# Performance work log

Hardware: AMD Instinct MI355X
Metric: run time of the kernel (lower is better)

The kernel has to match this reference:

```python
import jax, jax.numpy as jnp
import numpy as np

B, K, W = 16, 64, 2048
D, DH, DFF, NL, V = 512, 256, 2048, 4, 32001
LN_EPS = 1e-5


def _ln(x, g, b):
    mu = jnp.mean(x, axis=-1, keepdims=True)
    var = jnp.mean(jnp.square(x - mu), axis=-1, keepdims=True)
    return (x - mu) * jax.lax.rsqrt(var + LN_EPS) * g + b


def setup_inputs() -> dict:
    key = jax.random.key(0)
    ks = iter(jax.random.split(key, 64))
    nrm = lambda shape, s=0.02: (jax.random.normal(next(ks), shape, dtype=jnp.float32) * s)
    inp = {
        "cache": jax.random.randint(next(ks), (B, K), 0, V),
        "seq": jax.random.randint(next(ks), (B, W), 0, V),
        "item_embed": nrm((V, D)),
        "cache_pos_embed": nrm((K, D)),
        "seq_pos_embed": nrm((W, D)),
        "segment_embed": nrm((2, D)),
        # per-layer stacked params (leading dim NL)
        "wq_s": nrm((NL, D, DH)), "wk_s": nrm((NL, D, DH)), "wv_s": nrm((NL, D, DH)),
        "wq_c": nrm((NL, D, DH)), "wk_c": nrm((NL, D, DH)), "wv_c": nrm((NL, D, DH)),
        "w_out": nrm((NL, D, D)), "b_out": jnp.zeros((NL, D), jnp.float32),
        "ln1_g": jnp.ones((NL, D), jnp.float32), "ln1_b": jnp.zeros((NL, D), jnp.float32),
        "ln2_g": jnp.ones((NL, D), jnp.float32), "ln2_b": jnp.zeros((NL, D), jnp.float32),
        "w_ff1": nrm((NL, D, DFF)), "b_ff1": jnp.zeros((NL, DFF), jnp.float32),
        "w_ff2": nrm((NL, DFF, D)), "b_ff2": jnp.zeros((NL, D), jnp.float32),
        "fin_g": jnp.ones((D,), jnp.float32), "fin_b": jnp.zeros((D,), jnp.float32),
        "w_ev": nrm((D, 1)), "b_ev": jnp.zeros((1,), jnp.float32),
    }
    return inp


def _forward(cache, seq, item_embed, cache_pos_embed, seq_pos_embed, segment_embed,
             wq_s, wk_s, wv_s, wq_c, wk_c, wv_c, w_out, b_out,
             ln1_g, ln1_b, ln2_g, ln2_b, w_ff1, b_ff1, w_ff2, b_ff2,
             fin_g, fin_b, w_ev, b_ev):
    scale = 1.0 / jnp.sqrt(jnp.float32(DH))
    cache_emb = item_embed[cache] + cache_pos_embed[None, :, :] + segment_embed[0]
    seq_emb = item_embed[seq] + seq_pos_embed[None, :, :] + segment_embed[1]
    h = jnp.concatenate([cache_emb, seq_emb], axis=1)  # (B, K+W, D)
    L = K + W
    # additive mask for stream a: cache rows attend to all seq tokens,
    # seq rows are causal within the window.  (L, W)
    causal = jnp.triu(jnp.full((W, W), -jnp.inf, dtype=jnp.float32), k=1)
    mask_a = jnp.concatenate([jnp.zeros((K, W), jnp.float32), causal], axis=0)

    for l in range(NL):
        hn = _ln(h, ln1_g[l], ln1_b[l])
        hn_seq = hn[:, K:]
        hn_cache = hn[:, :K]
        # stream a: all tokens query the sequence window (causal for seq rows)
        q_a = hn @ wq_s[l]
        k_a = hn_seq @ wk_s[l]
        v_a = hn_seq @ wv_s[l]
        scores_a = jnp.einsum('bld,bwd->blw', q_a, k_a) * scale + mask_a
        out_a = jnp.einsum('blw,bwd->bld', jax.nn.softmax(scores_a, axis=-1), v_a)
        # stream b: all tokens query the cache slots (full attention)
        q_b = hn @ wq_c[l]
        k_b = hn_cache @ wk_c[l]
        v_b = hn_cache @ wv_c[l]
        scores_b = jnp.einsum('bld,bkd->blk', q_b, k_b) * scale
        out_b = jnp.einsum('blk,bkd->bld', jax.nn.softmax(scores_b, axis=-1), v_b)
        attn_out = jnp.concatenate([out_a, out_b], axis=-1)  # (B, L, D)
        h = h + attn_out @ w_out[l] + b_out[l]
        hn2 = _ln(h, ln2_g[l], ln2_b[l])
        h = h + jax.nn.relu(hn2 @ w_ff1[l] + b_ff1[l]) @ w_ff2[l] + b_ff2[l]

    h = _ln(h, fin_g, fin_b)
    logits = (h[:, :K] @ w_ev + b_ev)[..., 0]  # (B, K)
    return logits


def reference(cache, seq, item_embed, cache_pos_embed, seq_pos_embed, segment_embed,
              wq_s, wk_s, wv_s, wq_c, wk_c, wv_c, w_out, b_out,
              ln1_g, ln1_b, ln2_g, ln2_b, w_ff1, b_ff1, w_ff2, b_ff2,
              fin_g, fin_b, w_ev, b_ev):
    return _forward(cache, seq, item_embed, cache_pos_embed, seq_pos_embed, segment_embed,
                    wq_s, wk_s, wv_s, wq_c, wk_c, wv_c, w_out, b_out,
                    ln1_g, ln1_b, ln2_g, ln2_b, w_ff1, b_ff1, w_ff2, b_ff2,
                    fin_g, fin_b, w_ev, b_ev)
```

## Files before the change

### kernel.cpp

```cpp
#include <hip/hip_runtime.h>
#include <hip/hip_bf16.h>
#include <cstdint>

#define CB 16
#define CK 64
#define CW 2048
#define CL 2112
#define CD 512
#define CDH 256
#define CDFF 2048
#define CNL 4
#define CROWS (CB*CL)
#define RCH (CROWS/4)

typedef __attribute__((ext_vector_type(8))) short bf16x8;
typedef __attribute__((ext_vector_type(4))) float f32x4;

__device__ __forceinline__ float bf2f(unsigned short u) {
    union { unsigned int i; float f; } x; x.i = ((unsigned int)u) << 16; return x.f;
}

__device__ __forceinline__ void load_lds16(const void* g, void* l) {
    __builtin_amdgcn_global_load_lds(
        (const __attribute__((address_space(1))) void*)g,
        (__attribute__((address_space(3))) void*)l, 16, 0, 0);
}

__device__ __forceinline__ void xcd_swizzle(int& bx, int& by) {
    const int gx = gridDim.x, nwg = gx * gridDim.y;
    if ((nwg & 7) == 0) {
        const int flat = by * gx + bx;
        const int cpx = nwg >> 3;
        const int swz = (flat & 7) * cpx + (flat >> 3);
        bx = swz % gx; by = swz / gx;
    }
}

#define BM 128
#define BN 128
#define BKG 64

__global__ __launch_bounds__(256) void gemm_bt(
    const short* __restrict__ A, const short* __restrict__ Bt, void* __restrict__ C,
    const float* __restrict__ bias, int M, int N, int Kd,
    int lda, int ldb, int ldc, long sA, long sB, long sC, float scale, int epi,
    int ksplit)
{
    __shared__ short lA[2][BM * BKG];
    __shared__ short lB[2][BN * BKG];
    const int tid = threadIdx.x;
    const int wave = tid >> 6, lane = tid & 63;
    const int wy = wave >> 1, wx = wave & 1;
    const int lr = lane & 15, quad = lane >> 4;
    int bx = blockIdx.x, by = blockIdx.y;
    xcd_swizzle(bx, by);
    const int m0 = by * BM, n0 = bx * BN;
    const int z = blockIdx.z;
    const short* Ab = A + (size_t)z * sA;
    const short* Bb = Bt + (size_t)z * sB;

    f32x4 acc[4][4];
#pragma unroll
    for (int i = 0; i < 4; i++)
#pragma unroll
        for (int j = 0; j < 4; j++) acc[i][j] = (f32x4){0.f, 0.f, 0.f, 0.f};

    const int sRow = lane >> 3;
    const int sCol = (((lane & 7) ^ sRow) << 3);

    int kbeg = 0, kend = Kd;
    if (ksplit > 1) { const int kc = Kd / ksplit; kbeg = z * kc; kend = kbeg + kc; }
    const int nsteps = (kend - kbeg) / BKG;

    auto stage = [&](int buf, int k0) {
#pragma unroll
        for (int n = 0; n < 4; ++n) {
            const int c = wave * 4 + n;
            int ar = m0 + c * 8 + sRow; if (ar > M - 1) ar = M - 1;
            load_lds16(Ab + (size_t)ar * lda + k0 + sCol, &lA[buf][c * 512]);
            int br = n0 + c * 8 + sRow; if (br > N - 1) br = N - 1;
            load_lds16(Bb + (size_t)br * ldb + k0 + sCol, &lB[buf][c * 512]);
        }
    };

    stage(0, kbeg);
    for (int t = 0; t < nsteps; ++t) {
        const int cur = t & 1;
        if (t + 1 < nsteps) {
            stage(cur ^ 1, kbeg + (t + 1) * BKG);
            asm volatile("s_waitcnt vmcnt(8)\n\ts_barrier" ::: "memory");
        } else {
            asm volatile("s_waitcnt vmcnt(0)\n\ts_barrier" ::: "memory");
        }
#pragma unroll
        for (int kk = 0; kk < BKG; kk += 32) {
            const int k4 = kk >> 3;
            bf16x8 av[4], bv[4];
#pragma unroll
            for (int i = 0; i < 4; i++) {
                const int ri = wy * 64 + i * 16 + lr;
                av[i] = *(const bf16x8*)&lA[cur][ri * BKG + ((((k4 + quad) ^ (ri & 7)) << 3))];
            }
#pragma unroll
            for (int j = 0; j < 4; j++) {
                const int rj = wx * 64 + j * 16 + lr;
                bv[j] = *(const bf16x8*)&lB[cur][rj * BKG + ((((k4 + quad) ^ (rj & 7)) << 3))];
            }
#pragma unroll
            for (int i = 0; i < 4; i++)
#pragma unroll
                for (int j = 0; j < 4; j++)
                    acc[i][j] = __builtin_amdgcn_mfma_f32_16x16x32_bf16(av[i], bv[j], acc[i][j], 0, 0, 0);
        }
        asm volatile("s_barrier" ::: "memory");
    }

    const int colBase = n0 + wx * 64 + lr;
    if (epi == 3) {
        float* Cp = (float*)C + (size_t)z * sC;
#pragma unroll
        for (int i = 0; i < 4; i++) {
            const int row0 = m0 + wy * 64 + i * 16 + quad * 4;
#pragma unroll
            for (int j = 0; j < 4; j++) {
                const int col = colBase + j * 16;
                if (col >= N) continue;
                const float bv_ = bias ? bias[col] : 0.f;
#pragma unroll
                for (int r = 0; r < 4; r++) {
                    const int row = row0 + r;
                    if (row < M) Cp[(size_t)row * ldc + col] += acc[i][j][r] + bv_;
                }
            }
        }
    } else {
        __hip_bfloat16* Cp = (__hip_bfloat16*)C + (size_t)z * sC;
#pragma unroll
        for (int i = 0; i < 4; i++) {
            const int row0 = m0 + wy * 64 + i * 16 + quad * 4;
#pragma unroll
            for (int j = 0; j < 4; j++) {
                const int col = colBase + j * 16;
                if (col >= N) continue;
                const float bv_ = (epi == 1) ? bias[col] : 0.f;
#pragma unroll
                for (int r = 0; r < 4; r++) {
                    const int row = row0 + r;
                    if (row < M) {
                        float v = acc[i][j][r];
                        if (epi == 1) { v += bv_; v = v > 0.f ? v : 0.f; }
                        else if (epi == 2) v *= scale;
                        Cp[(size_t)row * ldc + col] = __float2bfloat16(v);
                    }
                }
            }
        }
    }
}

__global__ __launch_bounds__(256, 2) void flash_a(
    const short* __restrict__ q,
    const short* __restrict__ ka,
    const short* __restrict__ vt,
    short* __restrict__ out)
{
    __shared__ short kbuf[64 * 256];
    __shared__ short vbuf[256 * 64];
    __shared__ short pbuf[64 * 64];
    const int tid = threadIdx.x, wave = tid >> 6, lane = tid & 63;
    const int lr = lane & 15, quad = lane >> 4;

    const int id = blockIdx.x;
    const int x = id & 7, k = id >> 3;
    const int b = 2 * x + (k >= 33);
    const int mi = (k >= 33) ? (k - 33) : k;
    const int mt = (mi == 0) ? 0 : (33 - mi);
    const int m0 = mt * 64;
    const short* kab = ka + (size_t)b * 2048 * 256;
    const short* vtb = vt + (size_t)b * 256 * 2048;

    const int nkt = (mt == 0) ? 32 : mt;

    bf16x8 qf[8];
    {
        const int qr = m0 + wave * 16 + lr;
        const short* p0 = q + ((size_t)b * CL + qr) * 512;
#pragma unroll
        for (int s = 0; s < 8; ++s) qf[s] = *(const bf16x8*)(p0 + s * 32 + quad * 8);
    }

    auto stageK = [&](int kt) {
#pragma unroll
        for (int u = 0; u < 8; ++u) {
            const int seg = u * 4 + wave;
            const int idx = seg * 64 + lane;
            const int row = idx >> 5, cp = idx & 31;
            const int cs = cp ^ (row & 7);
            load_lds16(kab + (size_t)(kt * 64 + row) * 256 + cs * 8, kbuf + seg * 512);
        }
    };
    auto stageV = [&](int kt) {
#pragma unroll
        for (int u = 0; u < 8; ++u) {
            const int seg = u * 4 + wave;
            const int idx = seg * 64 + lane;
            const int row = idx >> 3, cp = idx & 7;
            const int cs = cp ^ (row & 7);
            load_lds16(vtb + (size_t)row * 2048 + kt * 64 + cs * 8, vbuf + seg * 512);
        }
    };

    f32x4 acc_o[16];
#pragma unroll
    for (int jd = 0; jd < 16; jd++) acc_o[jd] = (f32x4){0.f, 0.f, 0.f, 0.f};
    float m_run[4], l_run[4];
    int limit[4];
#pragma unroll
    for (int rr = 0; rr < 4; rr++) {
        m_run[rr] = -1e30f; l_run[rr] = 0.f;
        const int trow = m0 + wave * 16 + quad * 4 + rr;
        limit[rr] = (trow < CK) ? CW : (trow - (CK - 1));
    }

    for (int kt = 0; kt < nkt; ++kt) {
        stageK(kt);
        stageV(kt);
        __syncthreads();

        f32x4 s_[4];
#pragma unroll
        for (int j = 0; j < 4; j++) s_[j] = (f32x4){0.f, 0.f, 0.f, 0.f};
#pragma unroll
        for (int s = 0; s < 8; ++s) {
#pragma unroll
            for (int j = 0; j < 4; ++j) {
                const int rj = j * 16 + lr;
                const bf16x8 bv = *(const bf16x8*)&kbuf[rj * 256 + (((s * 4 + quad) ^ (rj & 7)) << 3)];
                s_[j] = __builtin_amdgcn_mfma_f32_16x16x32_bf16(qf[s], bv, s_[j], 0, 0, 0);
            }
        }

        const int kbase = kt * 64;
        float tmax[4];
#pragma unroll
        for (int rr = 0; rr < 4; rr++) tmax[rr] = -1e30f;
#pragma unroll
        for (int j = 0; j < 4; j++) {
            const int key = kbase + j * 16 + lr;
#pragma unroll
            for (int rr = 0; rr < 4; rr++) {
                const float v = (key < limit[rr]) ? s_[j][rr] * 0.0625f : -1e30f;
                s_[j][rr] = v;
                tmax[rr] = fmaxf(tmax[rr], v);
            }
        }
#pragma unroll
        for (int rr = 0; rr < 4; rr++) {
#pragma unroll
            for (int off = 1; off < 16; off <<= 1)
                tmax[rr] = fmaxf(tmax[rr], __shfl_xor(tmax[rr], off));
        }
        float scal[4], rowsum[4];
#pragma unroll
        for (int rr = 0; rr < 4; rr++) {
            const float mn = fmaxf(m_run[rr], tmax[rr]);
            scal[rr] = __expf(m_run[rr] - mn);
            m_run[rr] = mn;
            rowsum[rr] = 0.f;
        }
#pragma unroll
        for (int j = 0; j < 4; j++) {
            const int cch = j * 2 + (lr >> 3);
#pragma unroll
            for (int rr = 0; rr < 4; rr++) {
                const float e = __expf(s_[j][rr] - m_run[rr]);
                rowsum[rr] += e;
                const float eo = __shfl_xor(e, 1);
                const __hip_bfloat16 b0 = __float2bfloat16(e);
                const __hip_bfloat16 b1 = __float2bfloat16(eo);
                const unsigned pk = ((unsigned)(*(const unsigned short*)&b1) << 16)
                                  | (unsigned)(*(const unsigned short*)&b0);
                if (!(lane & 1)) {
                    const int prow = wave * 16 + quad * 4 + rr;
                    *(unsigned*)&pbuf[prow * 64 + ((cch ^ (prow & 7)) << 3) + (lr & 6)] = pk;
                }
            }
        }
#pragma unroll
        for (int rr = 0; rr < 4; rr++) {
#pragma unroll
            for (int off = 1; off < 16; off <<= 1)
                rowsum[rr] += __shfl_xor(rowsum[rr], off);
            l_run[rr] = l_run[rr] * scal[rr] + rowsum[rr];
        }
#pragma unroll
        for (int jd = 0; jd < 16; jd++)
#pragma unroll
            for (int rr = 0; rr < 4; rr++) acc_o[jd][rr] *= scal[rr];


        const int pr = wave * 16 + lr;
#pragma unroll
        for (int s2 = 0; s2 < 2; ++s2) {
            const bf16x8 pa = *(const bf16x8*)&pbuf[pr * 64 + (((s2 * 4 + quad) ^ (pr & 7)) << 3)];
#pragma unroll
            for (int jd = 0; jd < 16; ++jd) {
                const int rj = jd * 16 + lr;
                const bf16x8 bv = *(const bf16x8*)&vbuf[rj * 64 + (((s2 * 4 + quad) ^ (rj & 7)) << 3)];
                acc_o[jd] = __builtin_amdgcn_mfma_f32_16x16x32_bf16(pa, bv, acc_o[jd], 0, 0, 0);
            }
        }
        __syncthreads();
    }

#pragma unroll
    for (int rr = 0; rr < 4; rr++) {
        const int trow = m0 + wave * 16 + quad * 4 + rr;
        const float rinv = 1.f / l_run[rr];
        __hip_bfloat16* op = (__hip_bfloat16*)out + ((size_t)b * CL + trow) * CD;
#pragma unroll
        for (int jd = 0; jd < 16; jd++)
            op[jd * 16 + lr] = __float2bfloat16(acc_o[jd][rr] * rinv);
    }
}

__global__ void embed_kernel(const int* __restrict__ cache, const int* __restrict__ seq,
                             const float* __restrict__ item, const float* __restrict__ cpos,
                             const float* __restrict__ spos, const float* __restrict__ seg,
                             float* __restrict__ h)
{
    const int row = blockIdx.x;
    const int b = row / CL, t = row - b * CL;
    const int d = threadIdx.x * 4;
    int id; const float* pos; const float* sg;
    if (t < CK) { id = cache[b * CK + t]; pos = cpos + (size_t)t * CD; sg = seg; }
    else { const int tt = t - CK; id = seq[b * CW + tt]; pos = spos + (size_t)tt * CD; sg = seg + CD; }
    const float4 ev = *(const float4*)(item + (size_t)id * CD + d);
    const float4 pv = *(const float4*)(pos + d);
    const float4 sv = *(const float4*)(sg + d);
    float4 r; r.x = ev.x + pv.x + sv.x; r.y = ev.y + pv.y + sv.y;
    r.z = ev.z + pv.z + sv.z; r.w = ev.w + pv.w + sv.w;
    *(float4*)(h + (size_t)row * CD + d) = r;
}

__global__ __launch_bounds__(256) void ln_kernel(const float* __restrict__ h, const float* __restrict__ g,
                                                 const float* __restrict__ bb, __hip_bfloat16* __restrict__ out)
{
    const int row = blockIdx.x;
    const float* x = h + (size_t)row * CD;
    const int tid = threadIdx.x, wv = tid >> 6, lane = tid & 63;
    const float2 v = *(const float2*)(x + tid * 2);
    float s = v.x + v.y, s2 = v.x * v.x + v.y * v.y;
    __shared__ float red[8];
#pragma unroll
    for (int off = 32; off; off >>= 1) { s += __shfl_down(s, off); s2 += __shfl_down(s2, off); }
    if (lane == 0) { red[wv] = s; red[4 + wv] = s2; }
    __syncthreads();
    s = red[0] + red[1] + red[2] + red[3];
    s2 = red[4] + red[5] + red[6] + red[7];
    const float mu = s * (1.f / CD);
    const float var = s2 * (1.f / CD) - mu * mu;
    const float rs = rsqrtf(var + 1e-5f);
    const float2 gg = *(const float2*)(g + tid * 2);
    const float2 bv = *(const float2*)(bb + tid * 2);
    out[(size_t)row * CD + tid * 2 + 0] = __float2bfloat16((v.x - mu) * rs * gg.x + bv.x);
    out[(size_t)row * CD + tid * 2 + 1] = __float2bfloat16((v.y - mu) * rs * gg.y + bv.y);
}

__global__ __launch_bounds__(256) void softmax_b_kernel(__hip_bfloat16* __restrict__ sb)
{
    const int row = blockIdx.x * 4 + (threadIdx.x >> 6);
    const int lane = threadIdx.x & 63;
    __hip_bfloat16* pr = sb + (size_t)row * 64;
    float x = __bfloat162float(pr[lane]);
    float m = x;
#pragma unroll
    for (int off = 32; off; off >>= 1) m = fmaxf(m, __shfl_xor(m, off));
    const float e = __expf(x - m);
    float s = e;
#pragma unroll
    for (int off = 32; off; off >>= 1) s += __shfl_xor(s, off);
    pr[lane] = __float2bfloat16(e / s);
}

__global__ __launch_bounds__(256) void final_kernel(const float* __restrict__ h, const float* __restrict__ g,
                                                    const float* __restrict__ bb, const float* __restrict__ wev,
                                                    const float* __restrict__ bev, float* __restrict__ out)
{
    const int idx = blockIdx.x;
    const int b = idx >> 6, t = idx & 63;
    const float* x = h + ((size_t)b * CL + t) * CD;
    const int tid = threadIdx.x, wv = tid >> 6, lane = tid & 63;
    const float2 v = *(const float2*)(x + tid * 2);
    float s = v.x + v.y, s2 = v.x * v.x + v.y * v.y;
    __shared__ float red[8];
#pragma unroll
    for (int off = 32; off; off >>= 1) { s += __shfl_down(s, off); s2 += __shfl_down(s2, off); }
    if (lane == 0) { red[wv] = s; red[4 + wv] = s2; }
    __syncthreads();
    s = red[0] + red[1] + red[2] + red[3];
    s2 = red[4] + red[5] + red[6] + red[7];
    const float mu = s * (1.f / CD);
    const float var = s2 * (1.f / CD) - mu * mu;
    const float rs = rsqrtf(var + 1e-5f);
    const float2 gg = *(const float2*)(g + tid * 2);
    const float2 bv = *(const float2*)(bb + tid * 2);
    const float2 wv2 = *(const float2*)(wev + tid * 2);
    float val = ((v.x - mu) * rs * gg.x + bv.x) * wv2.x + ((v.y - mu) * rs * gg.y + bv.y) * wv2.y;
#pragma unroll
    for (int off = 32; off; off >>= 1) val += __shfl_down(val, off);
    __syncthreads();
    if (lane == 0) red[wv] = val;
    __syncthreads();
    if (tid == 0) out[idx] = red[0] + red[1] + red[2] + red[3] + bev[0];
}

__global__ void transpose_f32(const float* __restrict__ in, __hip_bfloat16* __restrict__ out,
                              int R, int Cc, long inzs, long outzs)
{
    __shared__ float tile[32][33];
    const size_t zi = (size_t)blockIdx.z * inzs;
    const size_t zo = (size_t)blockIdx.z * outzs;
    const int c0 = blockIdx.x * 32, r0 = blockIdx.y * 32;
    const int tx = threadIdx.x, ty = threadIdx.y;
#pragma unroll
    for (int i = ty; i < 32; i += 8)
        tile[i][tx] = in[zi + (size_t)(r0 + i) * Cc + c0 + tx];
    __syncthreads();
#pragma unroll
    for (int i = ty; i < 32; i += 8)
        out[zo + (size_t)(c0 + i) * R + r0 + tx] = __float2bfloat16(tile[tx][i]);
}

extern "C" void kernel_launch(void* const* d_in, const int* in_sizes, int n_in,
                              void* d_out, int out_size, void* d_ws, size_t ws_size,
                              hipStream_t stream)
{
    const int*   cache = (const int*)d_in[0];
    const int*   seq   = (const int*)d_in[1];
    const float* item  = (const float*)d_in[2];
    const float* cpos  = (const float*)d_in[3];
    const float* spos  = (const float*)d_in[4];
    const float* seg   = (const float*)d_in[5];
    const float* wq_s  = (const float*)d_in[6];
    const float* wk_s  = (const float*)d_in[7];
    const float* wv_s  = (const float*)d_in[8];
    const float* wq_c  = (const float*)d_in[9];
    const float* wk_c  = (const float*)d_in[10];
    const float* wv_c  = (const float*)d_in[11];
    const float* w_out = (const float*)d_in[12];
    const float* b_out = (const float*)d_in[13];
    const float* ln1_g = (const float*)d_in[14];
    const float* ln1_b = (const float*)d_in[15];
    const float* ln2_g = (const float*)d_in[16];
    const float* ln2_b = (const float*)d_in[17];
    const float* w_ff1 = (const float*)d_in[18];
    const float* b_ff1 = (const float*)d_in[19];
    const float* w_ff2 = (const float*)d_in[20];
    const float* b_ff2 = (const float*)d_in[21];
    const float* fin_g = (const float*)d_in[22];
    const float* fin_b = (const float*)d_in[23];
    const float* w_ev  = (const float*)d_in[24];
    const float* b_ev  = (const float*)d_in[25];

    char* p = (char*)d_ws;
    auto alloc = [&](size_t bytes) { char* r = p; p += (bytes + 255) & ~(size_t)255; return (void*)r; };
    float* h    = (float*)alloc((size_t)CROWS * CD * 4);
    short* hnat = (short*)alloc((size_t)CROWS * CD * 2);
    short* q    = (short*)alloc((size_t)CROWS * 512 * 2);
    short* ka   = (short*)alloc((size_t)CB * CW * CDH * 2);
    short* vt   = (short*)alloc((size_t)CB * CDH * CW * 2);
    short* kb   = (short*)alloc((size_t)CB * 64 * CDH * 2);
    short* vbT  = (short*)alloc((size_t)CB * CDH * 64 * 2);
    short* sb   = (short*)alloc((size_t)CB * CL * 64 * 2);
    short* big  = (short*)alloc((size_t)4 * CL * CW * 2);
    short* wqT  = (short*)alloc((size_t)CNL * 512 * CD * 2);
    short* wksT = (short*)alloc((size_t)CNL * CDH * CD * 2);
    short* wvsT = (short*)alloc((size_t)CNL * CDH * CD * 2);
    short* wkcT = (short*)alloc((size_t)CNL * CDH * CD * 2);
    short* wvcT = (short*)alloc((size_t)CNL * CDH * CD * 2);
    short* woT  = (short*)alloc((size_t)CNL * CD * CD * 2);
    short* wf1T = (short*)alloc((size_t)CNL * CDFF * CD * 2);
    short* wf2T = (short*)alloc((size_t)CNL * CD * CDFF * 2);

    const dim3 tb(32, 8);
    const long zqk = (long)CD * CDH;
    const long zqT = (long)512 * CD;
    transpose_f32<<<dim3(CDH/32, CD/32, CNL), tb, 0, stream>>>(wq_s, (__hip_bfloat16*)wqT, CD, CDH, zqk, zqT);
    transpose_f32<<<dim3(CDH/32, CD/32, CNL), tb, 0, stream>>>(wq_c, (__hip_bfloat16*)(wqT + (size_t)CDH * CD), CD, CDH, zqk, zqT);
    transpose_f32<<<dim3(CDH/32, CD/32, CNL), tb, 0, stream>>>(wk_s, (__hip_bfloat16*)wksT, CD, CDH, zqk, zqk);
    transpose_f32<<<dim3(CDH/32, CD/32, CNL), tb, 0, stream>>>(wv_s, (__hip_bfloat16*)wvsT, CD, CDH, zqk, zqk);
    transpose_f32<<<dim3(CDH/32, CD/32, CNL), tb, 0, stream>>>(wk_c, (__hip_bfloat16*)wkcT, CD, CDH, zqk, zqk);
    transpose_f32<<<dim3(CDH/32, CD/32, CNL), tb, 0, stream>>>(wv_c, (__hip_bfloat16*)wvcT, CD, CDH, zqk, zqk);
    transpose_f32<<<dim3(CD/32, CD/32, CNL), tb, 0, stream>>>(w_out, (__hip_bfloat16*)woT, CD, CD, (long)CD*CD, (long)CD*CD);
    transpose_f32<<<dim3(CDFF/32, CD/32, CNL), tb, 0, stream>>>(w_ff1, (__hip_bfloat16*)wf1T, CD, CDFF, (long)CD*CDFF, (long)CD*CDFF);
    transpose_f32<<<dim3(CD/32, CDFF/32, CNL), tb, 0, stream>>>(w_ff2, (__hip_bfloat16*)wf2T, CDFF, CD, (long)CD*CDFF, (long)CD*CDFF);

    embed_kernel<<<CROWS, 128, 0, stream>>>(cache, seq, item, cpos, spos, seg, h);

    const int mtilesR = CROWS / 128;
    const int mtilesL = (CL + 127) / 128;

    for (int l = 0; l < CNL; ++l) {
        const short* wqTl  = wqT  + (size_t)l * 512 * CD;
        const short* wksTl = wksT + (size_t)l * CDH * CD;
        const short* wvsTl = wvsT + (size_t)l * CDH * CD;
        const short* wkcTl = wkcT + (size_t)l * CDH * CD;
        const short* wvcTl = wvcT + (size_t)l * CDH * CD;
        const short* woTl  = woT  + (size_t)l * CD * CD;
        const short* wf1Tl = wf1T + (size_t)l * CDFF * CD;
        const short* wf2Tl = wf2T + (size_t)l * CD * CDFF;

        ln_kernel<<<CROWS, 256, 0, stream>>>(h, ln1_g + l * CD, ln1_b + l * CD, (__hip_bfloat16*)hnat);

        gemm_bt<<<dim3(512/128, mtilesR, 1), 256, 0, stream>>>(hnat, wqTl, q, nullptr,
            CROWS, 512, CD, CD, CD, 512, 0, 0, 0, 1.f, 0, 1);
        gemm_bt<<<dim3(CDH/128, CW/128, CB), 256, 0, stream>>>(hnat + (size_t)CK * CD, wksTl, ka, nullptr,
            CW, CDH, CD, CD, CD, CDH, (long)CL * CD, 0, (long)CW * CDH, 1.f, 0, 1);
        gemm_bt<<<dim3(CDH/128, 1, CB), 256, 0, stream>>>(hnat, wkcTl, kb, nullptr,
            64, CDH, CD, CD, CD, CDH, (long)CL * CD, 0, (long)64 * CDH, 1.f, 0, 1);
        gemm_bt<<<dim3(1, CDH/128, CB), 256, 0, stream>>>(wvcTl, hnat, vbT, nullptr,
            CDH, 64, CD, CD, CD, 64, 0, (long)CL * CD, (long)CDH * 64, 1.f, 0, 1);
        gemm_bt<<<dim3(CW/128, CDH/128, CB), 256, 0, stream>>>(wvsTl, hnat + (size_t)CK * CD, vt, nullptr,
            CDH, CW, CD, CD, CD, CW, 0, (long)CL * CD, (long)CDH * CW, 1.f, 0, 1);

        gemm_bt<<<dim3(1, mtilesL, CB), 256, 0, stream>>>(q + CDH, kb, sb, nullptr,
            CL, 64, CDH, 512, CDH, 64, (long)CL * 512, (long)64 * CDH, (long)CL * 64, 0.0625f, 2, 1);
        softmax_b_kernel<<<(CB * CL) / 4, 256, 0, stream>>>((__hip_bfloat16*)sb);
        gemm_bt<<<dim3(CDH/128, mtilesL, CB), 256, 0, stream>>>(sb, vbT, hnat + CDH, nullptr,
            CL, CDH, 64, 64, 64, CD, (long)CL * 64, (long)CDH * 64, (long)CL * CD, 1.f, 0, 1);

        flash_a<<<dim3(528), 256, 0, stream>>>(q, ka, vt, hnat);

        gemm_bt<<<dim3(CD/128, mtilesR, 1), 256, 0, stream>>>(hnat, woTl, h, b_out + l * CD,
            CROWS, CD, CD, CD, CD, CD, 0, 0, 0, 1.f, 3, 1);

        ln_kernel<<<CROWS, 256, 0, stream>>>(h, ln2_g + l * CD, ln2_b + l * CD, (__hip_bfloat16*)hnat);

        for (int c = 0; c < 4; ++c) {
            const size_t r0 = (size_t)c * RCH;
            gemm_bt<<<dim3(CDFF/128, RCH/128, 1), 256, 0, stream>>>(hnat + r0 * CD, wf1Tl, big, b_ff1 + l * CDFF,
                RCH, CDFF, CD, CD, CD, CDFF, 0, 0, 0, 1.f, 1, 1);
            gemm_bt<<<dim3(CD/128, RCH/128, 1), 256, 0, stream>>>(big, wf2Tl, h + r0 * CD, b_ff2 + l * CD,
                RCH, CD, CDFF, CDFF, CDFF, CD, 0, 0, 0, 1.f, 3, 1);
        }
    }

    final_kernel<<<CB * CK, 256, 0, stream>>>(h, fin_g, fin_b, w_ev, b_ev, (float*)d_out);
}
```

Measured before the change: 3.675 ms.

## Read K/V directly from global in flash attention with smaller 32-row blocks

Removes the LDS staging buffers for K and V in the stream-a flash attention kernel. Each wave now loads its MFMA operands directly from global memory, which also removes the per-tile barriers. The query tile shrinks from 64 to 32 rows, with 2 waves per block and twice as many blocks, to improve occupancy and causal load balance. The cost is that K/V data is no longer shared through LDS, so each wave fetches it separately through the caches with less-coalesced 16-byte row accesses.

New measurement: 4.955 ms. 34.8% more time.

```diff
diff --git a/kernel.cpp b/kernel.cpp
--- a/kernel.cpp
+++ b/kernel.cpp
@@ -158,28 +158,26 @@
     }
 }
 
-__global__ __launch_bounds__(256, 2) void flash_a(
+__global__ __launch_bounds__(128, 3) void flash_a(
     const short* __restrict__ q,
     const short* __restrict__ ka,
     const short* __restrict__ vt,
     short* __restrict__ out)
 {
-    __shared__ short kbuf[64 * 256];
-    __shared__ short vbuf[256 * 64];
-    __shared__ short pbuf[64 * 64];
+    __shared__ short pbuf[32 * 64];
     const int tid = threadIdx.x, wave = tid >> 6, lane = tid & 63;
     const int lr = lane & 15, quad = lane >> 4;
 
     const int id = blockIdx.x;
     const int x = id & 7, k = id >> 3;
-    const int b = 2 * x + (k >= 33);
-    const int mi = (k >= 33) ? (k - 33) : k;
-    const int mt = (mi == 0) ? 0 : (33 - mi);
-    const int m0 = mt * 64;
+    const int b = 2 * x + (k >= 66);
+    const int kk = (k >= 66) ? (k - 66) : k;
+    const int mt = (kk < 2) ? kk : (67 - kk);
+    const int m0 = mt * 32;
     const short* kab = ka + (size_t)b * 2048 * 256;
     const short* vtb = vt + (size_t)b * 256 * 2048;
 
-    const int nkt = (mt == 0) ? 32 : mt;
+    const int nkt = (mt < 2) ? 32 : ((mt * 32 + 31) >> 6);
 
     bf16x8 qf[8];
     {
@@ -189,27 +187,6 @@
         for (int s = 0; s < 8; ++s) qf[s] = *(const bf16x8*)(p0 + s * 32 + quad * 8);
     }
 
-    auto stageK = [&](int kt) {
-#pragma unroll
-        for (int u = 0; u < 8; ++u) {
-            const int seg = u * 4 + wave;
-            const int idx = seg * 64 + lane;
-            const int row = idx >> 5, cp = idx & 31;
-            const int cs = cp ^ (row & 7);
-            load_lds16(kab + (size_t)(kt * 64 + row) * 256 + cs * 8, kbuf + seg * 512);
-        }
-    };
-    auto stageV = [&](int kt) {
-#pragma unroll
-        for (int u = 0; u < 8; ++u) {
-            const int seg = u * 4 + wave;
-            const int idx = seg * 64 + lane;
-            const int row = idx >> 3, cp = idx & 7;
-            const int cs = cp ^ (row & 7);
-            load_lds16(vtb + (size_t)row * 2048 + kt * 64 + cs * 8, vbuf + seg * 512);
-        }
-    };
-
     f32x4 acc_o[16];
 #pragma unroll
     for (int jd = 0; jd < 16; jd++) acc_o[jd] = (f32x4){0.f, 0.f, 0.f, 0.f};
@@ -223,21 +200,19 @@
     }
 
     for (int kt = 0; kt < nkt; ++kt) {
-        stageK(kt);
-        stageV(kt);
-        __syncthreads();
-
+        const short* kp = kab + (size_t)(kt * 64 + lr) * 256 + quad * 8;
         f32x4 s_[4];
 #pragma unroll
         for (int j = 0; j < 4; j++) s_[j] = (f32x4){0.f, 0.f, 0.f, 0.f};
 #pragma unroll
         for (int s = 0; s < 8; ++s) {
-#pragma unroll
-            for (int j = 0; j < 4; ++j) {
-                const int rj = j * 16 + lr;
-                const bf16x8 bv = *(const bf16x8*)&kbuf[rj * 256 + (((s * 4 + quad) ^ (rj & 7)) << 3)];
-                s_[j] = __builtin_amdgcn_mfma_f32_16x16x32_bf16(qf[s], bv, s_[j], 0, 0, 0);
-            }
+            bf16x8 bv[4];
+#pragma unroll
+            for (int j = 0; j < 4; ++j)
+                bv[j] = *(const bf16x8*)(kp + (size_t)j * 16 * 256 + s * 32);
+#pragma unroll
+            for (int j = 0; j < 4; ++j)
+                s_[j] = __builtin_amdgcn_mfma_f32_16x16x32_bf16(qf[s], bv[j], s_[j], 0, 0, 0);
         }
 
         const int kbase = kt * 64;
@@ -298,19 +273,17 @@
 #pragma unroll
             for (int rr = 0; rr < 4; rr++) acc_o[jd][rr] *= scal[rr];
 
-
         const int pr = wave * 16 + lr;
+        const short* vp = vtb + (size_t)lr * 2048 + kt * 64 + quad * 8;
 #pragma unroll
         for (int s2 = 0; s2 < 2; ++s2) {
             const bf16x8 pa = *(const bf16x8*)&pbuf[pr * 64 + (((s2 * 4 + quad) ^ (pr & 7)) << 3)];
 #pragma unroll
             for (int jd = 0; jd < 16; ++jd) {
-                const int rj = jd * 16 + lr;
-                const bf16x8 bv = *(const bf16x8*)&vbuf[rj * 64 + (((s2 * 4 + quad) ^ (rj & 7)) << 3)];
+                const bf16x8 bv = *(const bf16x8*)(vp + (size_t)jd * 16 * 2048 + s2 * 32);
                 acc_o[jd] = __builtin_amdgcn_mfma_f32_16x16x32_bf16(pa, bv, acc_o[jd], 0, 0, 0);
             }
         }
-        __syncthreads();
     }
 
 #pragma unroll
@@ -530,7 +503,7 @@
         gemm_bt<<<dim3(CDH/128, mtilesL, CB), 256, 0, stream>>>(sb, vbT, hnat + CDH, nullptr,
             CL, CDH, 64, 64, 64, CD, (long)CL * 64, (long)CDH * 64, (long)CL * CD, 1.f, 0, 1);
 
-        flash_a<<<dim3(528), 256, 0, stream>>>(q, ka, vt, hnat);
+        flash_a<<<dim3(1056), 128, 0, stream>>>(q, ka, vt, hnat);
 
         gemm_bt<<<dim3(CD/128, mtilesR, 1), 256, 0, stream>>>(hnat, woTl, h, b_out + l * CD,
             CROWS, CD, CD, CD, CD, CD, 0, 0, 0, 1.f, 3, 1);
```
